# Kernel optimization log

Hardware: AMD Instinct MI355X
Metric: run time of the kernel (lower is better)

## Reference

```python
import jax, jax.numpy as jnp
import numpy as np

L = 128          # bandlimit (max_l)
NTHETA = 256     # Gauss-Legendre latitudes (>= L for exact quadrature)
NPHI = 512       # longitudes (>= 2L-1)
C_IN, C_OUT = 32, 32


def _normalized_assoc_legendre(Lmax, xg):
    """Pbar_lm(x) with Condon-Shortley phase, orthonormal on the sphere.
    Returns (Lmax, Lmax, T) for m>=0; zero for m>l."""
    T = xg.shape[0]
    P = np.zeros((Lmax, Lmax, T), dtype=np.float64)
    sx = np.sqrt(np.maximum(1.0 - xg * xg, 0.0))
    P[0, 0] = 1.0 / np.sqrt(4.0 * np.pi)
    for m in range(1, Lmax):
        P[m, m] = -np.sqrt((2 * m + 1) / (2.0 * m)) * sx * P[m - 1, m - 1]
    for m in range(0, Lmax - 1):
        P[m + 1, m] = np.sqrt(2 * m + 3.0) * xg * P[m, m]
    for m in range(Lmax):
        for l in range(m + 2, Lmax):
            a = np.sqrt((4.0 * l * l - 1.0) / (l * l - m * m))
            b = np.sqrt(((l - 1.0) ** 2 - m * m) / (4.0 * (l - 1.0) ** 2 - 1.0))
            P[l, m] = a * (xg * P[l - 1, m] - b * P[l - 2, m])
    return P


def _build_basis():
    # Gauss-Legendre quadrature in cos(theta): exact for degree <= 2*NTHETA-1
    xg, wg = np.polynomial.legendre.leggauss(NTHETA)
    P = _normalized_assoc_legendre(L, xg)  # (L, L, T), m>=0
    # Full basis B[l, m+L-1, t]; Pbar_{l,-m} = (-1)^m Pbar_{l,m}
    B = np.zeros((L, 2 * L - 1, NTHETA), dtype=np.float64)
    for m in range(-(L - 1), L):
        B[:, m + L - 1, :] = ((-1.0) ** abs(m) if m < 0 else 1.0) * P[:, abs(m), :]
    return B.astype(np.float32), wg.astype(np.float32)


def setup_inputs() -> dict:
    key = jax.random.key(0)
    k1, k2, k3 = jax.random.split(key, 3)
    x = jax.random.normal(k1, (NTHETA, NPHI, C_IN), dtype=jnp.float32)
    std = 1.0 / (C_IN + C_OUT)
    wr = std * jax.random.normal(k2, (L, 2 * L - 1, C_IN, C_OUT), dtype=jnp.float32)
    wi = std * jax.random.normal(k3, (L, 2 * L - 1, C_IN, C_OUT), dtype=jnp.float32)
    B, wg = _build_basis()
    return {"x": x, "weights_real": wr, "weights_imag": wi,
            "legendre": jnp.asarray(B), "quad_w": jnp.asarray(wg)}


def reference(x, weights_real, weights_imag, legendre, quad_w):
    ntheta, nphi, _ = x.shape
    Lb = legendre.shape[0]
    # --- forward SHT (per channel, vectorized) ---
    # longitude FFT: Fm[t,k,c] = sum_p x e^{-i 2pi k p / nphi}; dphi = 2pi/nphi
    Fm = jnp.fft.fft(x.astype(jnp.complex64), axis=1) * (2.0 * np.pi / nphi)
    midx = np.arange(-(Lb - 1), Lb) % nphi            # FFT bins for m=-(L-1)..L-1
    Fm_sel = Fm[:, midx, :]                           # (t, 2L-1, c)
    Bw = legendre * quad_w[None, None, :]             # quadrature-weighted basis
    # flm[l,m,c] = sum_t w_t Pbar_lm(theta_t) Fm[t,m,c]
    flm = jnp.einsum('lmt,tmc->lmc', Bw.astype(jnp.complex64), Fm_sel)
    # --- spectral conv: per-(l,m) channel mixing ---
    W = weights_real.astype(jnp.complex64) + 1j * weights_imag.astype(jnp.complex64)
    y = jnp.einsum('lmc,lmco->lmo', flm, W)           # (L, 2L-1, O)
    # --- inverse SHT ---
    G = jnp.einsum('lmt,lmo->tmo', legendre.astype(jnp.complex64), y)  # (t, 2L-1, O)
    spec = jnp.zeros((ntheta, nphi, G.shape[-1]), dtype=jnp.complex64)
    spec = spec.at[:, midx, :].set(G)
    out = jnp.fft.ifft(spec, axis=1) * nphi           # f = sum_m G e^{i m phi}
    return jnp.moveaxis(out.real, 2, 0)               # (O, ntheta, nphi)
```

## Files before the change

### kernel.cpp

```cpp
#include <hip/hip_runtime.h>
#include <math.h>

#define DEVFN __global__ __launch_bounds__(256)

namespace {
constexpr int LL  = 128;
constexpr int MM2 = 255;
constexpr int NT  = 256;
constexpr int NP  = 512;
constexpr int NC  = 32;
constexpr int NO  = 32;
constexpr float TWO_PI = 6.283185307179586476925286766559f;
}

DEVFN void k0_twiddle(float* __restrict__ tw1, float* __restrict__ tw5c,
                      float* __restrict__ tw5s) {
  const int idx = blockIdx.x * 256 + threadIdx.x;
  const float phi = TWO_PI / (float)NP;
  const float fscale = TWO_PI / (float)NP;
  if (idx < NP * 256) {
    const int p = idx >> 8;
    const int n = idx & 255;
    const int m = n >> 1;
    const int k = (m * p) & (NP - 1);
    float s, c;
    sincosf(phi * (float)k, &s, &c);
    tw1[idx] = (n & 1) ? (-s * fscale) : (c * fscale);
  }
  if (idx < LL * NP) {
    const int m = idx >> 9;
    const int p = idx & (NP - 1);
    const int k = (m * p) & (NP - 1);
    float s, c;
    sincosf(phi * (float)k, &s, &c);
    tw5c[idx] = c;
    tw5s[idx] = s;
  }
}

DEVFN void k1_dft(const float* __restrict__ x, const float* __restrict__ tw1,
                  const float* __restrict__ wg,
                  float* __restrict__ fwr, float* __restrict__ fwi) {
  __shared__ float As[32][64];
  __shared__ float Bs[32][64];
  const int r0 = blockIdx.x * 64;
  const int n0 = blockIdx.y * 64;
  const int tid = threadIdx.x;
  const int tx = tid & 15, ty = tid >> 4;
  float acc[4][4] = {};
  for (int p0 = 0; p0 < NP; p0 += 32) {
#pragma unroll
    for (int i = 0; i < 8; ++i) {
      const int idx = tid + i * 256;
      const int k = idx >> 6, rl = idx & 63;
      const int r = r0 + rl;
      As[k][rl] = x[((r >> 5) * NP + p0 + k) * NC + (r & 31)];
      Bs[k][rl] = tw1[(p0 + k) * 256 + n0 + rl];
    }
    __syncthreads();
#pragma unroll
    for (int k = 0; k < 32; ++k) {
      float a[4], b[4];
      *(float4*)a = *(const float4*)&As[k][ty * 4];
      *(float4*)b = *(const float4*)&Bs[k][tx * 4];
#pragma unroll
      for (int i = 0; i < 4; ++i)
#pragma unroll
        for (int j = 0; j < 4; ++j) acc[i][j] = fmaf(a[i], b[j], acc[i][j]);
    }
    __syncthreads();
  }
#pragma unroll
  for (int i = 0; i < 4; ++i) {
    const int r = r0 + ty * 4 + i;
    const int t = r >> 5, c = r & 31;
    const float w = wg[t];
#pragma unroll
    for (int j = 0; j < 4; ++j) {
      const int n = n0 + tx * 4 + j;
      const int m = n >> 1;
      float* dst = (n & 1) ? fwi : fwr;
      dst[(m * NT + t) * NC + c] = acc[i][j] * w;
    }
  }
}

DEVFN void k2_flm(const float* __restrict__ leg, const float* __restrict__ fwr,
                  const float* __restrict__ fwi, float* __restrict__ flr,
                  float* __restrict__ fli) {
  const int m = blockIdx.x;
  const int l = m + blockIdx.y * 8 + (threadIdx.x >> 5);
  const int c = threadIdx.x & 31;
  if (l >= LL) return;
  const float* lg = leg + ((size_t)(l * MM2 + 127 + m)) * NT;
  const float* fr = fwr + (size_t)m * NT * NC + c;
  const float* fi = fwi + (size_t)m * NT * NC + c;
  float ar = 0.f, ai = 0.f;
  for (int t = 0; t < NT; t += 4) {
#pragma unroll
    for (int u = 0; u < 4; ++u) {
      const float b = lg[t + u];
      ar = fmaf(b, fr[(t + u) * NC], ar);
      ai = fmaf(b, fi[(t + u) * NC], ai);
    }
  }
  flr[(m * LL + l) * NC + c] = ar;
  fli[(m * LL + l) * NC + c] = ai;
}

DEVFN void k3_y(const float* __restrict__ wr, const float* __restrict__ wi,
                const float* __restrict__ flr, const float* __restrict__ fli,
                float* __restrict__ ya, float* __restrict__ yb) {
  const int m = blockIdx.x;
  const int lbase = m + (int)blockIdx.y * 32;
  if (lbase >= LL) return;
  __shared__ float sfr[32][33];
  __shared__ float sfi[32][33];
  const int tid = threadIdx.x;
  for (int i = tid; i < 1024; i += 256) {
    const int lr = i >> 5, cc = i & 31;
    const int l = lbase + lr;
    sfr[lr][cc] = (l < LL) ? flr[(m * LL + l) * NC + cc] : 0.f;
    sfi[lr][cc] = (l < LL) ? fli[(m * LL + l) * NC + cc] : 0.f;
  }
  __syncthreads();
  const int lo = tid >> 3;
  const int o4 = (tid & 7) << 2;
  const int l = lbase + lo;
  if (l >= LL) return;
  const float s0 = (m > 0) ? 1.0f : 0.0f;
  const size_t base_p = ((size_t)(l * MM2 + 127 + m) * NC) * NO + o4;
  const size_t base_n = ((size_t)(l * MM2 + 127 - m) * NC) * NO + o4;
  float ax = 0, ay = 0, az = 0, aw = 0;
  float bx = 0, by = 0, bz = 0, bw = 0;
#pragma unroll 4
  for (int c = 0; c < NC; ++c) {
    const float fr = sfr[lo][c], fi = sfi[lo][c];
    const float4 pr = *(const float4*)(wr + base_p + c * NO);
    const float4 nr = *(const float4*)(wr + base_n + c * NO);
    const float4 pi = *(const float4*)(wi + base_p + c * NO);
    const float4 ni = *(const float4*)(wi + base_n + c * NO);
    const float wax = pr.x + s0 * nr.x, way = pr.y + s0 * nr.y,
                waz = pr.z + s0 * nr.z, waw = pr.w + s0 * nr.w;
    const float wbx = s0 * ni.x - pi.x, wby = s0 * ni.y - pi.y,
                wbz = s0 * ni.z - pi.z, wbw = s0 * ni.w - pi.w;
    ax = fmaf(fr, wax, fmaf(fi, wbx, ax));
    ay = fmaf(fr, way, fmaf(fi, wby, ay));
    az = fmaf(fr, waz, fmaf(fi, wbz, az));
    aw = fmaf(fr, waw, fmaf(fi, wbw, aw));
    bx = fmaf(fr, wbx, fmaf(-fi, wax, bx));
    by = fmaf(fr, wby, fmaf(-fi, way, by));
    bz = fmaf(fr, wbz, fmaf(-fi, waz, bz));
    bw = fmaf(fr, wbw, fmaf(-fi, waw, bw));
  }
  float4 va = {ax, ay, az, aw}, vb = {bx, by, bz, bw};
  *(float4*)(ya + (size_t)(m * LL + l) * NO + o4) = va;
  *(float4*)(yb + (size_t)(m * LL + l) * NO + o4) = vb;
}

DEVFN void k4_G(const float* __restrict__ leg, const float* __restrict__ ya,
                const float* __restrict__ yb, float* __restrict__ Aa,
                float* __restrict__ Bb) {
  const int m = blockIdx.x;
  const int o = threadIdx.x & 31;
  const int tq = threadIdx.x >> 5;
  const int t0 = blockIdx.y * 32 + tq * 4;
  float aa[4] = {}, bb[4] = {};
  for (int l = m; l < LL; ++l) {
    const float* lgl = leg + ((size_t)(l * MM2 + 127 + m)) * NT + t0;
    const float yav = ya[(m * LL + l) * NO + o];
    const float ybv = yb[(m * LL + l) * NO + o];
#pragma unroll
    for (int i = 0; i < 4; ++i) {
      const float g = lgl[i];
      aa[i] = fmaf(g, yav, aa[i]);
      bb[i] = fmaf(g, ybv, bb[i]);
    }
  }
#pragma unroll
  for (int i = 0; i < 4; ++i) {
    Aa[(size_t)(m * NT + t0 + i) * NO + o] = aa[i];
    Bb[(size_t)(m * NT + t0 + i) * NO + o] = bb[i];
  }
}

DEVFN void k5_idft(const float* __restrict__ Aa, const float* __restrict__ Bb,
                   const float* __restrict__ twc, const float* __restrict__ tws,
                   float* __restrict__ out) {
  __shared__ float Asm[16][64];
  __shared__ float Bsm[16][64];
  __shared__ float Csm[16][128];
  __shared__ float Ssm[16][128];
  const int r0 = blockIdx.x * 64;
  const int p0 = blockIdx.y * 128;
  const int tid = threadIdx.x;
  const int tx = tid & 15, ty = tid >> 4;
  float acc[4][8] = {};
  for (int m0 = 0; m0 < LL; m0 += 16) {
#pragma unroll
    for (int i = 0; i < 4; ++i) {
      const int idx = tid + i * 256;
      const int k = idx >> 6, rl = idx & 63;
      Asm[k][rl] = Aa[(size_t)(m0 + k) * 8192 + r0 + rl];
      Bsm[k][rl] = Bb[(size_t)(m0 + k) * 8192 + r0 + rl];
    }
#pragma unroll
    for (int i = 0; i < 8; ++i) {
      const int idx = tid + i * 256;
      const int k = idx >> 7, pl = idx & 127;
      Csm[k][pl] = twc[(m0 + k) * NP + p0 + pl];
      Ssm[k][pl] = tws[(m0 + k) * NP + p0 + pl];
    }
    __syncthreads();
#pragma unroll
    for (int k = 0; k < 16; ++k) {
      float a[4], b[4], cc[8], ss[8];
      *(float4*)a = *(const float4*)&Asm[k][ty * 4];
      *(float4*)b = *(const float4*)&Bsm[k][ty * 4];
      *(float4*)&cc[0] = *(const float4*)&Csm[k][tx * 4];
      *(float4*)&cc[4] = *(const float4*)&Csm[k][64 + tx * 4];
      *(float4*)&ss[0] = *(const float4*)&Ssm[k][tx * 4];
      *(float4*)&ss[4] = *(const float4*)&Ssm[k][64 + tx * 4];
#pragma unroll
      for (int jr = 0; jr < 4; ++jr)
#pragma unroll
        for (int jp = 0; jp < 8; ++jp)
          acc[jr][jp] = fmaf(a[jr], cc[jp], fmaf(b[jr], ss[jp], acc[jr][jp]));
    }
    __syncthreads();
  }
#pragma unroll
  for (int jr = 0; jr < 4; ++jr) {
    const int r = r0 + ty * 4 + jr;
    const int t = r >> 5, o = r & 31;
    float* op = out + ((size_t)o * NT + t) * NP + p0;
#pragma unroll
    for (int jp = 0; jp < 8; ++jp) {
      const int pl = (jp < 4) ? (tx * 4 + jp) : (64 + tx * 4 + (jp - 4));
      op[pl] = acc[jr][jp];
    }
  }
}

extern "C" void kernel_launch(void* const* d_in, const int* in_sizes, int n_in,
                              void* d_out, int out_size, void* d_ws, size_t ws_size,
                              hipStream_t stream) {
  const float* x   = (const float*)d_in[0];
  const float* wr  = (const float*)d_in[1];
  const float* wi  = (const float*)d_in[2];
  const float* leg = (const float*)d_in[3];
  const float* wg  = (const float*)d_in[4];
  float* out = (float*)d_out;

  float* ws   = (float*)d_ws;
  float* tw1  = ws;
  float* tw5c = tw1 + 131072;
  float* tw5s = tw5c + 65536;
  float* fwr  = tw5s + 65536;
  float* fwi  = fwr + 1048576;
  float* flr  = fwi + 1048576;
  float* fli  = flr + 524288;
  float* ya   = fli + 524288;
  float* yb   = ya + 524288;
  float* Aa   = fwr;
  float* Bb   = fwi;

  hipLaunchKernelGGL(k0_twiddle, dim3(512), dim3(256), 0, stream, tw1, tw5c, tw5s);
  hipLaunchKernelGGL(k1_dft, dim3(128, 4), dim3(256), 0, stream, x, tw1, wg, fwr, fwi);
  hipLaunchKernelGGL(k2_flm, dim3(128, 16), dim3(256), 0, stream, leg, fwr, fwi, flr, fli);
  hipLaunchKernelGGL(k3_y, dim3(128, 4), dim3(256), 0, stream, wr, wi, flr, fli, ya, yb);
  hipLaunchKernelGGL(k4_G, dim3(128, 8), dim3(256), 0, stream, leg, ya, yb, Aa, Bb);
  hipLaunchKernelGGL(k5_idft, dim3(128, 4), dim3(256), 0, stream, Aa, Bb, tw5c, tw5s, out);
}
```

Baseline: 442.5 us.

## Run forward and inverse DFT GEMMs on bf16 MFMA with transposed operands

Replaces the two FP32 SIMT GEMMs (the longitude DFT and inverse DFT) with bf16 MFMA 16x16x32 kernels. Twiddles, the input (via a new transpose/convert kernel) and the intermediate G are stored as bf16 in K-contiguous layouts, and the inverse GEMM folds the cos and sin terms into a single K=256 dimension. The aim is to cut the FP32 FMA cost of the DFT stages, at the price of an extra transpose pass and reduced precision that may hurt accuracy.

Result: faster. 405.6 us (-8.3%).

```diff
diff --git a/kernel.cpp b/kernel.cpp
--- a/kernel.cpp
+++ b/kernel.cpp
@@ -13,74 +13,112 @@
 constexpr float TWO_PI = 6.283185307179586476925286766559f;
 }
 
-DEVFN void k0_twiddle(float* __restrict__ tw1, float* __restrict__ tw5c,
-                      float* __restrict__ tw5s) {
+typedef short v8s __attribute__((ext_vector_type(8)));
+typedef float v4f __attribute__((ext_vector_type(4)));
+
+__device__ inline unsigned short f2bf(float f) {
+  unsigned int u = __float_as_uint(f);
+  return (unsigned short)((u + 0x7FFFu + ((u >> 16) & 1u)) >> 16);
+}
+
+DEVFN void k0_twiddle(unsigned short* __restrict__ tw1t, unsigned short* __restrict__ vt) {
   const int idx = blockIdx.x * 256 + threadIdx.x;
   const float phi = TWO_PI / (float)NP;
-  const float fscale = TWO_PI / (float)NP;
-  if (idx < NP * 256) {
-    const int p = idx >> 8;
-    const int n = idx & 255;
+  const float fs  = TWO_PI / (float)NP;
+  {
+    const int n = idx >> 9, p = idx & 511;
     const int m = n >> 1;
     const int k = (m * p) & (NP - 1);
     float s, c;
     sincosf(phi * (float)k, &s, &c);
-    tw1[idx] = (n & 1) ? (-s * fscale) : (c * fscale);
-  }
-  if (idx < LL * NP) {
-    const int m = idx >> 9;
-    const int p = idx & (NP - 1);
-    const int k = (m * p) & (NP - 1);
+    tw1t[idx] = f2bf((n & 1) ? (-s * fs) : (c * fs));
+  }
+  {
+    const int p = idx >> 8, k = idx & 255;
+    const int m = k >> 1;
+    const int kk = (m * p) & (NP - 1);
     float s, c;
-    sincosf(phi * (float)k, &s, &c);
-    tw5c[idx] = c;
-    tw5s[idx] = s;
-  }
-}
-
-DEVFN void k1_dft(const float* __restrict__ x, const float* __restrict__ tw1,
-                  const float* __restrict__ wg,
-                  float* __restrict__ fwr, float* __restrict__ fwi) {
-  __shared__ float As[32][64];
-  __shared__ float Bs[32][64];
-  const int r0 = blockIdx.x * 64;
-  const int n0 = blockIdx.y * 64;
+    sincosf(phi * (float)kk, &s, &c);
+    vt[idx] = f2bf((k & 1) ? s : c);
+  }
+}
+
+DEVFN void k0b_xpose(const float* __restrict__ x, unsigned short* __restrict__ xb) {
+  __shared__ float sm[32][65];
+  const int t = blockIdx.x;
+  const int p0 = blockIdx.y * 64;
   const int tid = threadIdx.x;
-  const int tx = tid & 15, ty = tid >> 4;
-  float acc[4][4] = {};
-  for (int p0 = 0; p0 < NP; p0 += 32) {
-#pragma unroll
-    for (int i = 0; i < 8; ++i) {
-      const int idx = tid + i * 256;
-      const int k = idx >> 6, rl = idx & 63;
-      const int r = r0 + rl;
-      As[k][rl] = x[((r >> 5) * NP + p0 + k) * NC + (r & 31)];
-      Bs[k][rl] = tw1[(p0 + k) * 256 + n0 + rl];
+#pragma unroll
+  for (int i = 0; i < 8; ++i) {
+    const int idx = tid + i * 256;
+    const int p = idx >> 5, c = idx & 31;
+    sm[c][p] = x[((size_t)t * NP + p0 + p) * NC + c];
+  }
+  __syncthreads();
+  const int c = tid >> 3, pg = tid & 7;
+  unsigned short pk[8];
+#pragma unroll
+  for (int u = 0; u < 8; ++u) pk[u] = f2bf(sm[c][pg * 8 + u]);
+  *(uint4*)(xb + ((size_t)(t * 32 + c)) * NP + p0 + pg * 8) = *(const uint4*)pk;
+}
+
+DEVFN void k1_mfma(const unsigned short* __restrict__ xb,
+                   const unsigned short* __restrict__ tw1t,
+                   const float* __restrict__ wg,
+                   float* __restrict__ fwr, float* __restrict__ fwi) {
+  __shared__ unsigned short As[128 * 32];
+  __shared__ unsigned short Bs[128 * 32];
+  const int tid = threadIdx.x;
+  const int r0 = blockIdx.x * 128;
+  const int n0 = blockIdx.y * 128;
+  const int wid = tid >> 6, lane = tid & 63;
+  const int wm = wid & 1, wn = wid >> 1;
+  v4f acc[4][4];
+#pragma unroll
+  for (int i = 0; i < 4; ++i)
+#pragma unroll
+    for (int j = 0; j < 4; ++j) {
+      acc[i][j][0] = 0.f; acc[i][j][1] = 0.f; acc[i][j][2] = 0.f; acc[i][j][3] = 0.f;
+    }
+  const int lr = lane & 15, lk = (lane >> 4) * 8;
+  for (int k0 = 0; k0 < 512; k0 += 32) {
+#pragma unroll
+    for (int s = 0; s < 2; ++s) {
+      const int chunk = tid + s * 256;
+      const int row = chunk >> 2, c16 = chunk & 3;
+      *(uint4*)&As[row * 32 + c16 * 8] =
+          *(const uint4*)&xb[(size_t)(r0 + row) * 512 + k0 + c16 * 8];
+      *(uint4*)&Bs[row * 32 + c16 * 8] =
+          *(const uint4*)&tw1t[(size_t)(n0 + row) * 512 + k0 + c16 * 8];
     }
     __syncthreads();
-#pragma unroll
-    for (int k = 0; k < 32; ++k) {
-      float a[4], b[4];
-      *(float4*)a = *(const float4*)&As[k][ty * 4];
-      *(float4*)b = *(const float4*)&Bs[k][tx * 4];
-#pragma unroll
-      for (int i = 0; i < 4; ++i)
-#pragma unroll
-        for (int j = 0; j < 4; ++j) acc[i][j] = fmaf(a[i], b[j], acc[i][j]);
-    }
+    v8s af[4], bf[4];
+#pragma unroll
+    for (int i = 0; i < 4; ++i) af[i] = *(const v8s*)&As[(wm * 64 + i * 16 + lr) * 32 + lk];
+#pragma unroll
+    for (int j = 0; j < 4; ++j) bf[j] = *(const v8s*)&Bs[(wn * 64 + j * 16 + lr) * 32 + lk];
+#pragma unroll
+    for (int i = 0; i < 4; ++i)
+#pragma unroll
+      for (int j = 0; j < 4; ++j)
+        acc[i][j] = __builtin_amdgcn_mfma_f32_16x16x32_bf16(af[i], bf[j], acc[i][j], 0, 0, 0);
     __syncthreads();
   }
+  const int lrow = (lane >> 4) * 4;
 #pragma unroll
   for (int i = 0; i < 4; ++i) {
-    const int r = r0 + ty * 4 + i;
-    const int t = r >> 5, c = r & 31;
-    const float w = wg[t];
+    const int rbase = r0 + wm * 64 + i * 16 + lrow;
 #pragma unroll
     for (int j = 0; j < 4; ++j) {
-      const int n = n0 + tx * 4 + j;
-      const int m = n >> 1;
+      const int n = n0 + wn * 64 + j * 16 + lr;
+      const int mI = n >> 1;
       float* dst = (n & 1) ? fwi : fwr;
-      dst[(m * NT + t) * NC + c] = acc[i][j] * w;
+#pragma unroll
+      for (int reg = 0; reg < 4; ++reg) {
+        const int r = rbase + reg;
+        const int t = r >> 5, c = r & 31;
+        dst[((size_t)mI * NT + t) * NC + c] = acc[i][j][reg] * wg[t];
+      }
     }
   }
 }
@@ -118,10 +156,10 @@
   __shared__ float sfi[32][33];
   const int tid = threadIdx.x;
   for (int i = tid; i < 1024; i += 256) {
-    const int lr = i >> 5, cc = i & 31;
-    const int l = lbase + lr;
-    sfr[lr][cc] = (l < LL) ? flr[(m * LL + l) * NC + cc] : 0.f;
-    sfi[lr][cc] = (l < LL) ? fli[(m * LL + l) * NC + cc] : 0.f;
+    const int lr2 = i >> 5, cc = i & 31;
+    const int l = lbase + lr2;
+    sfr[lr2][cc] = (l < LL) ? flr[(m * LL + l) * NC + cc] : 0.f;
+    sfi[lr2][cc] = (l < LL) ? fli[(m * LL + l) * NC + cc] : 0.f;
   }
   __syncthreads();
   const int lo = tid >> 3;
@@ -159,8 +197,7 @@
 }
 
 DEVFN void k4_G(const float* __restrict__ leg, const float* __restrict__ ya,
-                const float* __restrict__ yb, float* __restrict__ Aa,
-                float* __restrict__ Bb) {
+                const float* __restrict__ yb, unsigned short* __restrict__ ut) {
   const int m = blockIdx.x;
   const int o = threadIdx.x & 31;
   const int tq = threadIdx.x >> 5;
@@ -179,65 +216,65 @@
   }
 #pragma unroll
   for (int i = 0; i < 4; ++i) {
-    Aa[(size_t)(m * NT + t0 + i) * NO + o] = aa[i];
-    Bb[(size_t)(m * NT + t0 + i) * NO + o] = bb[i];
-  }
-}
-
-DEVFN void k5_idft(const float* __restrict__ Aa, const float* __restrict__ Bb,
-                   const float* __restrict__ twc, const float* __restrict__ tws,
+    const unsigned int pk = (unsigned int)f2bf(aa[i]) | ((unsigned int)f2bf(bb[i]) << 16);
+    *(unsigned int*)&ut[((size_t)((t0 + i) * 32 + o)) * 256 + 2 * m] = pk;
+  }
+}
+
+DEVFN void k5_mfma(const unsigned short* __restrict__ ut,
+                   const unsigned short* __restrict__ vt,
                    float* __restrict__ out) {
-  __shared__ float Asm[16][64];
-  __shared__ float Bsm[16][64];
-  __shared__ float Csm[16][128];
-  __shared__ float Ssm[16][128];
-  const int r0 = blockIdx.x * 64;
+  __shared__ unsigned short As[128 * 32];
+  __shared__ unsigned short Bs[128 * 32];
+  const int tid = threadIdx.x;
+  const int r0 = blockIdx.x * 128;
   const int p0 = blockIdx.y * 128;
-  const int tid = threadIdx.x;
-  const int tx = tid & 15, ty = tid >> 4;
-  float acc[4][8] = {};
-  for (int m0 = 0; m0 < LL; m0 += 16) {
-#pragma unroll
-    for (int i = 0; i < 4; ++i) {
-      const int idx = tid + i * 256;
-      const int k = idx >> 6, rl = idx & 63;
-      Asm[k][rl] = Aa[(size_t)(m0 + k) * 8192 + r0 + rl];
-      Bsm[k][rl] = Bb[(size_t)(m0 + k) * 8192 + r0 + rl];
-    }
-#pragma unroll
-    for (int i = 0; i < 8; ++i) {
-      const int idx = tid + i * 256;
-      const int k = idx >> 7, pl = idx & 127;
-      Csm[k][pl] = twc[(m0 + k) * NP + p0 + pl];
-      Ssm[k][pl] = tws[(m0 + k) * NP + p0 + pl];
+  const int wid = tid >> 6, lane = tid & 63;
+  const int wm = wid & 1, wn = wid >> 1;
+  v4f acc[4][4];
+#pragma unroll
+  for (int i = 0; i < 4; ++i)
+#pragma unroll
+    for (int j = 0; j < 4; ++j) {
+      acc[i][j][0] = 0.f; acc[i][j][1] = 0.f; acc[i][j][2] = 0.f; acc[i][j][3] = 0.f;
+    }
+  const int lr = lane & 15, lk = (lane >> 4) * 8;
+  for (int k0 = 0; k0 < 256; k0 += 32) {
+#pragma unroll
+    for (int s = 0; s < 2; ++s) {
+      const int chunk = tid + s * 256;
+      const int row = chunk >> 2, c16 = chunk & 3;
+      *(uint4*)&As[row * 32 + c16 * 8] =
+          *(const uint4*)&ut[(size_t)(r0 + row) * 256 + k0 + c16 * 8];
+      *(uint4*)&Bs[row * 32 + c16 * 8] =
+          *(const uint4*)&vt[(size_t)(p0 + row) * 256 + k0 + c16 * 8];
     }
     __syncthreads();
-#pragma unroll
-    for (int k = 0; k < 16; ++k) {
-      float a[4], b[4], cc[8], ss[8];
-      *(float4*)a = *(const float4*)&Asm[k][ty * 4];
-      *(float4*)b = *(const float4*)&Bsm[k][ty * 4];
-      *(float4*)&cc[0] = *(const float4*)&Csm[k][tx * 4];
-      *(float4*)&cc[4] = *(const float4*)&Csm[k][64 + tx * 4];
-      *(float4*)&ss[0] = *(const float4*)&Ssm[k][tx * 4];
-      *(float4*)&ss[4] = *(const float4*)&Ssm[k][64 + tx * 4];
-#pragma unroll
-      for (int jr = 0; jr < 4; ++jr)
-#pragma unroll
-        for (int jp = 0; jp < 8; ++jp)
-          acc[jr][jp] = fmaf(a[jr], cc[jp], fmaf(b[jr], ss[jp], acc[jr][jp]));
-    }
+    v8s af[4], bf[4];
+#pragma unroll
+    for (int i = 0; i < 4; ++i) af[i] = *(const v8s*)&As[(wm * 64 + i * 16 + lr) * 32 + lk];
+#pragma unroll
+    for (int j = 0; j < 4; ++j) bf[j] = *(const v8s*)&Bs[(wn * 64 + j * 16 + lr) * 32 + lk];
+#pragma unroll
+    for (int i = 0; i < 4; ++i)
+#pragma unroll
+      for (int j = 0; j < 4; ++j)
+        acc[i][j] = __builtin_amdgcn_mfma_f32_16x16x32_bf16(af[i], bf[j], acc[i][j], 0, 0, 0);
     __syncthreads();
   }
-#pragma unroll
-  for (int jr = 0; jr < 4; ++jr) {
-    const int r = r0 + ty * 4 + jr;
-    const int t = r >> 5, o = r & 31;
-    float* op = out + ((size_t)o * NT + t) * NP + p0;
-#pragma unroll
-    for (int jp = 0; jp < 8; ++jp) {
-      const int pl = (jp < 4) ? (tx * 4 + jp) : (64 + tx * 4 + (jp - 4));
-      op[pl] = acc[jr][jp];
+  const int lrow = (lane >> 4) * 4;
+#pragma unroll
+  for (int i = 0; i < 4; ++i) {
+    const int rbase = r0 + wm * 64 + i * 16 + lrow;
+#pragma unroll
+    for (int j = 0; j < 4; ++j) {
+      const int p = p0 + wn * 64 + j * 16 + lr;
+#pragma unroll
+      for (int reg = 0; reg < 4; ++reg) {
+        const int r = rbase + reg;
+        const int t = r >> 5, o = r & 31;
+        out[((size_t)o * NT + t) * NP + p] = acc[i][j][reg];
+      }
     }
   }
 }
@@ -252,23 +289,22 @@
   const float* wg  = (const float*)d_in[4];
   float* out = (float*)d_out;
 
-  float* ws   = (float*)d_ws;
-  float* tw1  = ws;
-  float* tw5c = tw1 + 131072;
-  float* tw5s = tw5c + 65536;
-  float* fwr  = tw5s + 65536;
-  float* fwi  = fwr + 1048576;
-  float* flr  = fwi + 1048576;
-  float* fli  = flr + 524288;
-  float* ya   = fli + 524288;
-  float* yb   = ya + 524288;
-  float* Aa   = fwr;
-  float* Bb   = fwi;
-
-  hipLaunchKernelGGL(k0_twiddle, dim3(512), dim3(256), 0, stream, tw1, tw5c, tw5s);
-  hipLaunchKernelGGL(k1_dft, dim3(128, 4), dim3(256), 0, stream, x, tw1, wg, fwr, fwi);
+  unsigned short* tw1t = (unsigned short*)d_ws;
+  unsigned short* vt   = tw1t + 131072;
+  unsigned short* xb   = vt + 131072;
+  unsigned short* ut   = xb + 4194304;
+  float* fwr = (float*)(ut + 2097152);
+  float* fwi = fwr + 1048576;
+  float* flr = fwi + 1048576;
+  float* fli = flr + 524288;
+  float* ya  = fli + 524288;
+  float* yb  = ya + 524288;
+
+  hipLaunchKernelGGL(k0_twiddle, dim3(512), dim3(256), 0, stream, tw1t, vt);
+  hipLaunchKernelGGL(k0b_xpose, dim3(256, 8), dim3(256), 0, stream, x, xb);
+  hipLaunchKernelGGL(k1_mfma, dim3(64, 2), dim3(256), 0, stream, xb, tw1t, wg, fwr, fwi);
   hipLaunchKernelGGL(k2_flm, dim3(128, 16), dim3(256), 0, stream, leg, fwr, fwi, flr, fli);
   hipLaunchKernelGGL(k3_y, dim3(128, 4), dim3(256), 0, stream, wr, wi, flr, fli, ya, yb);
-  hipLaunchKernelGGL(k4_G, dim3(128, 8), dim3(256), 0, stream, leg, ya, yb, Aa, Bb);
-  hipLaunchKernelGGL(k5_idft, dim3(128, 4), dim3(256), 0, stream, Aa, Bb, tw5c, tw5s, out);
-}
+  hipLaunchKernelGGL(k4_G, dim3(128, 8), dim3(256), 0, stream, leg, ya, yb, ut);
+  hipLaunchKernelGGL(k5_mfma, dim3(64, 4), dim3(256), 0, stream, ut, vt, out);
+}
```
